# Kernel optimization log

Measured on AMD Instinct MI355X. Metric: run time of the kernel, lower is better.

Reference implementation:

```python
import jax, jax.numpy as jnp
import numpy as np

TOP_K = 2
EPS = 1e-20


def setup_inputs() -> dict:
    key = jax.random.key(0)
    ks = jax.random.split(key, 8)
    B, S, H, E, D = 4, 2048, 1024, 8, 2048
    s = 0.02
    return {
        "x":  jax.random.normal(ks[0], (B, S, H), dtype=jnp.float32),
        "Wr": jax.random.normal(ks[1], (H, E), dtype=jnp.float32) * s,
        "Wg": jax.random.normal(ks[2], (E, H, D), dtype=jnp.float32) * s,
        "Wu": jax.random.normal(ks[3], (E, H, D), dtype=jnp.float32) * s,
        "Wd": jax.random.normal(ks[4], (E, D, H), dtype=jnp.float32) * s,
        "Sg": jax.random.normal(ks[5], (H, D), dtype=jnp.float32) * s,
        "Su": jax.random.normal(ks[6], (H, D), dtype=jnp.float32) * s,
        "Sd": jax.random.normal(ks[7], (D, H), dtype=jnp.float32) * s,
    }


def reference(x, Wr, Wg, Wu, Wd, Sg, Su, Sd):
    B, S, H = x.shape
    T = B * S
    xt = x.reshape(T, H)

    # Router: softmax scores, top-k, renormalize top-k weights
    scores = jax.nn.softmax(xt @ Wr, axis=-1)            # [T, E]
    topk_w, topk_idx = jax.lax.top_k(scores, TOP_K)      # [T, K]
    topk_w = topk_w / (topk_w.sum(axis=-1, keepdims=True) + EPS)

    # Per-expert SwiGLU FFN computed densely over all tokens (vectorized over E)
    g = jax.nn.silu(jnp.einsum('th,ehd->etd', xt, Wg))   # [E, T, D]
    u = jnp.einsum('th,ehd->etd', xt, Wu)                # [E, T, D]
    out_all = jnp.einsum('etd,edh->eth', g * u, Wd)      # [E, T, H]

    # Combine: gather each token's top-k expert outputs, weighted sum
    tok = jnp.arange(T)[:, None]                          # [T, 1]
    gathered = out_all[topk_idx, tok, :]                  # [T, K, H]
    out = jnp.sum(gathered * topk_w[..., None], axis=1).reshape(B, S, H)

    # Shared expert (applied to original input, added to MoE output)
    shared = (jax.nn.silu(x @ Sg) * (x @ Su)) @ Sd        # [B, S, H]
    return out + shared
```

## Files before the change

kernel.cpp:

```cpp
#include <hip/hip_runtime.h>
#include <stdint.h>

#define T_TOK 8192
#define HD 1024
#define ED 8
#define DD 2048
#define BM 128
#define BK 32
#define TILE_SHARED 64
#define TILE_MAX 200
#define ROWCAP 25600
#define RT_TPW 8

typedef short short8 __attribute__((ext_vector_type(8)));
typedef unsigned short ushort8 __attribute__((ext_vector_type(8)));
typedef float f32x4 __attribute__((ext_vector_type(4)));

__device__ __forceinline__ unsigned short f2bf(float f) {
  union { float f; unsigned int u; } v; v.f = f;
  unsigned int r = (v.u + 0x7fffu + ((v.u >> 16) & 1u)) >> 16;
  return (unsigned short)r;
}

__device__ __forceinline__ void gll16(const void* g, void* l) {
  __builtin_amdgcn_global_load_lds(
      (const __attribute__((address_space(1))) unsigned int*)g,
      (__attribute__((address_space(3))) unsigned int*)l, 16, 0, 0);
}

__global__ __launch_bounds__(256) void k_zero(float* __restrict__ outp) {
  size_t i = (size_t)blockIdx.x * 256 + threadIdx.x;
  ((float4*)outp)[i] = make_float4(0.f, 0.f, 0.f, 0.f);
}

__global__ __launch_bounds__(256) void k_init(int* counts, int* tok, float* wrow) {
  int i = blockIdx.x * 256 + threadIdx.x;
  if (i < 32) counts[i] = 0;
  if (i < ROWCAP) {
    tok[i] = (i < T_TOK) ? i : 0;
    wrow[i] = (i < T_TOK) ? 1.0f : 0.0f;
  }
}

__global__ __launch_bounds__(256) void k_transpose(const float* __restrict__ in,
    unsigned short* __restrict__ outp, int R, int C) {
  __shared__ float tile[64][65];
  size_t boff = (size_t)blockIdx.z * (size_t)R * (size_t)C;
  in += boff; outp += boff;
  int c0 = blockIdx.x * 64, r0 = blockIdx.y * 64;
  int tid = threadIdx.x;
  int lr = tid >> 4;
  int lc = (tid & 15) << 2;
#pragma unroll
  for (int p = 0; p < 4; ++p) {
    int row = lr + p * 16;
    float4 v = *(const float4*)&in[(size_t)(r0 + row) * C + c0 + lc];
    tile[row][lc] = v.x; tile[row][lc + 1] = v.y;
    tile[row][lc + 2] = v.z; tile[row][lc + 3] = v.w;
  }
  __syncthreads();
  int cc = tid >> 2;
#pragma unroll
  for (int p = 0; p < 2; ++p) {
    int g = (tid & 3) + p * 4;
    int rr = g * 8;
    ushort8 v;
#pragma unroll
    for (int q = 0; q < 8; ++q) v[q] = f2bf(tile[rr + q][cc]);
    *(ushort8*)&outp[(size_t)(c0 + cc) * R + r0 + rr] = v;
  }
}

__global__ __launch_bounds__(256) void k_router(const float* __restrict__ x,
    const float* __restrict__ Wr, unsigned short* __restrict__ xb,
    int* __restrict__ counts, int* __restrict__ topE, float* __restrict__ topW) {
  __shared__ float wrT[ED * HD];
  __shared__ int hist[ED];
  int tid = threadIdx.x;
  if (tid < ED) hist[tid] = 0;
  for (int i = tid; i < ED * HD; i += 256) {
    int e = i >> 10, h = i & (HD - 1);
    wrT[i] = Wr[h * ED + e];
  }
  __syncthreads();
  int lane = tid & 63, wave = tid >> 6;
  int tbase = (blockIdx.x * 4 + wave) * RT_TPW;
  for (int tt = 0; tt < RT_TPW; ++tt) {
    int t = tbase + tt;
    const float* xrow = x + (size_t)t * HD;
    unsigned short* xbrow = xb + (size_t)t * HD;
    float acc[ED] = {0, 0, 0, 0, 0, 0, 0, 0};
#pragma unroll
    for (int i = 0; i < HD / 64; ++i) {
      int h = i * 64 + lane;
      float v = xrow[h];
      xbrow[h] = f2bf(v);
#pragma unroll
      for (int e = 0; e < ED; ++e) acc[e] += v * wrT[e * HD + h];
    }
#pragma unroll
    for (int off = 32; off; off >>= 1)
#pragma unroll
      for (int e = 0; e < ED; ++e) acc[e] += __shfl_xor(acc[e], off);
    if (lane == 0) {
      float m = acc[0];
#pragma unroll
      for (int e = 1; e < ED; ++e) m = fmaxf(m, acc[e]);
      float p[ED], s = 0.f;
#pragma unroll
      for (int e = 0; e < ED; ++e) { p[e] = __expf(acc[e] - m); s += p[e]; }
      int i0 = 0;
#pragma unroll
      for (int e = 1; e < ED; ++e) if (acc[e] > acc[i0]) i0 = e;
      int i1 = -1;
#pragma unroll
      for (int e = 0; e < ED; ++e) {
        if (e == i0) continue;
        if (i1 < 0 || acc[e] > acc[i1]) i1 = e;
      }
      float p0 = p[i0] / s, p1 = p[i1] / s;
      float rs = p0 + p1 + 1e-20f;
      topE[t * 2] = i0; topE[t * 2 + 1] = i1;
      topW[t * 2] = p0 / rs; topW[t * 2 + 1] = p1 / rs;
      atomicAdd(&hist[i0], 1);
      atomicAdd(&hist[i1], 1);
    }
  }
  __syncthreads();
  if (tid < ED) atomicAdd(&counts[tid], hist[tid]);
}

__global__ __launch_bounds__(256) void k_plan(const int* __restrict__ counts, int* cursor,
    int* __restrict__ tileE, int* __restrict__ tileEnd) {
  __shared__ int tstart[ED + 1], segend[ED];
  if (threadIdx.x == 0) {
    int base = T_TOK, rt = TILE_SHARED;
    for (int e = 0; e < ED; ++e) {
      int c = counts[e];
      cursor[e] = base;
      tstart[e] = rt;
      segend[e] = base + c;
      int tiles = (c + BM - 1) >> 7;
      rt += tiles;
      base += tiles << 7;
    }
    tstart[ED] = rt;
  }
  __syncthreads();
  for (int rt = threadIdx.x; rt < TILE_MAX; rt += 256) {
    int e = -1, end = 0;
    if (rt < TILE_SHARED) { e = ED; end = T_TOK; }
    else {
      for (int q = 0; q < ED; ++q)
        if (rt >= tstart[q] && rt < tstart[q + 1]) { e = q; end = segend[q]; }
    }
    tileE[rt] = e; tileEnd[rt] = end;
  }
}

__global__ __launch_bounds__(256) void k_scatter(const int* __restrict__ topE,
    const float* __restrict__ topW, int* cursor, int* tok, float* wrow) {
  __shared__ int lcount[ED], lbase[ED];
  int tid = threadIdx.x;
  if (tid < ED) lcount[tid] = 0;
  __syncthreads();
  int t = blockIdx.x * 256 + tid;
  int e0 = topE[t * 2], e1 = topE[t * 2 + 1];
  float w0 = topW[t * 2], w1 = topW[t * 2 + 1];
  int s0 = atomicAdd(&lcount[e0], 1);
  int s1 = atomicAdd(&lcount[e1], 1);
  __syncthreads();
  if (tid < ED) lbase[tid] = atomicAdd(&cursor[tid], lcount[tid]);
  __syncthreads();
  int p0 = lbase[e0] + s0;
  int p1 = lbase[e1] + s1;
  tok[p0] = t; wrow[p0] = w0;
  tok[p1] = t; wrow[p1] = w1;
}


__global__ __launch_bounds__(256, 3) void k_gemm1(
    const unsigned short* __restrict__ xb,
    const unsigned short* __restrict__ wgt, const unsigned short* __restrict__ wut,
    const unsigned short* __restrict__ sgt, const unsigned short* __restrict__ sut,
    const int* __restrict__ tok, const int* __restrict__ tileE,
    const int* __restrict__ tileEnd, unsigned short* __restrict__ hbuf, int tileBase) {
  int lin = blockIdx.y * 32 + blockIdx.x;
  int q = (32 * gridDim.y) >> 3;
  int wk = (lin & 7) * q + (lin >> 3);
  int bx = wk & 31, by = wk >> 5;

  int lt = by;
  int rt = tileBase + lt;
  int e = tileE[rt];
  if (e < 0) return;
  int n0 = bx * 64;
  int grow0 = rt * BM;
  int hrow0 = lt * BM;
  int segEnd = tileEnd[rt];
  const unsigned short* bg = (e == ED) ? sgt : wgt + (size_t)e * DD * HD;
  const unsigned short* bu = (e == ED) ? sut : wut + (size_t)e * DD * HD;

  __shared__ __align__(16) unsigned short As[3][BM * BK];
  __shared__ __align__(16) unsigned short Bg[3][64 * BK];
  __shared__ __align__(16) unsigned short Bu[3][64 * BK];

  int tid = threadIdx.x, lane = tid & 63, wave = tid >> 6;
  int wm = (wave & 1) * 64, wn = (wave >> 1) * 32;
  int kc = (lane & 3) ^ ((lane >> 3) & 3);
  int rl = lane >> 2;

  int ldsA[2];
  const unsigned short* pA[2];
#pragma unroll
  for (int r = 0; r < 2; ++r) {
    int chunk = r * 4 + wave;
    ldsA[r] = chunk * 512;
    pA[r] = xb + (size_t)tok[grow0 + chunk * 16 + rl] * HD + kc * 8;
  }
  const unsigned short* pG = bg + (size_t)(n0 + wave * 16 + rl) * HD + kc * 8;
  const unsigned short* pU = bu + (size_t)(n0 + wave * 16 + rl) * HD + kc * 8;
  int dB = wave * 512;

  f32x4 zero = {0.f, 0.f, 0.f, 0.f};
  f32x4 accg[4][2], accu[4][2];
#pragma unroll
  for (int i = 0; i < 4; ++i)
#pragma unroll
    for (int j = 0; j < 2; ++j) { accg[i][j] = zero; accu[i][j] = zero; }

  int m15 = lane & 15;
  int sl8 = (((lane >> 4) ^ ((lane >> 1) & 3)) * 8);

  gll16(pA[0],      &As[0][ldsA[0]]);
  gll16(pA[1],      &As[0][ldsA[1]]);
  gll16(pG,         &Bg[0][dB]);
  gll16(pU,         &Bu[0][dB]);
  __builtin_amdgcn_sched_barrier(0);
  gll16(pA[0] + BK, &As[1][ldsA[0]]);
  gll16(pA[1] + BK, &As[1][ldsA[1]]);
  gll16(pG + BK,    &Bg[1][dB]);
  gll16(pU + BK,    &Bu[1][dB]);

  const int NT = HD / BK;
  for (int t = 0; t < NT; ++t) {
    int b = t % 3;
    if (t + 1 < NT) asm volatile("s_waitcnt vmcnt(4)" ::: "memory");
    else            asm volatile("s_waitcnt vmcnt(0)" ::: "memory");
    __builtin_amdgcn_sched_barrier(0);
    __builtin_amdgcn_s_barrier();
    __builtin_amdgcn_sched_barrier(0);
    int k2 = (t + 2) * BK;
    if (k2 < HD) {
      int b2 = (t + 2) % 3;
      gll16(pA[0] + k2, &As[b2][ldsA[0]]);
      gll16(pA[1] + k2, &As[b2][ldsA[1]]);
      gll16(pG + k2,    &Bg[b2][dB]);
      gll16(pU + k2,    &Bu[b2][dB]);
    }
    __builtin_amdgcn_sched_barrier(0);
    short8 af[4], bgf[2], buf_[2];
#pragma unroll
    for (int i = 0; i < 4; ++i)
      af[i] = *(const short8*)(&As[b][(wm + i * 16 + m15) * BK + sl8]);
#pragma unroll
    for (int j = 0; j < 2; ++j) {
      bgf[j]  = *(const short8*)(&Bg[b][(wn + j * 16 + m15) * BK + sl8]);
      buf_[j] = *(const short8*)(&Bu[b][(wn + j * 16 + m15) * BK + sl8]);
    }
#pragma unroll
    for (int i = 0; i < 4; ++i)
#pragma unroll
      for (int j = 0; j < 2; ++j) {
        accg[i][j] = __builtin_amdgcn_mfma_f32_16x16x32_bf16(af[i], bgf[j],  accg[i][j], 0, 0, 0);
        accu[i][j] = __builtin_amdgcn_mfma_f32_16x16x32_bf16(af[i], buf_[j], accu[i][j], 0, 0, 0);
      }
    __builtin_amdgcn_sched_barrier(0);
  }

  int colB = n0 + wn + m15;
  int rowB = wm + ((lane >> 4) << 2);
#pragma unroll
  for (int i = 0; i < 4; ++i)
#pragma unroll
    for (int j = 0; j < 2; ++j)
#pragma unroll
      for (int r = 0; r < 4; ++r) {
        int lr = rowB + i * 16 + r;
        float g = accg[i][j][r], u = accu[i][j][r];
        float h = (grow0 + lr < segEnd) ? (g / (1.0f + __expf(-g))) * u : 0.0f;
        hbuf[(size_t)(hrow0 + lr) * DD + colB + j * 16] = f2bf(h);
      }
}

__global__ __launch_bounds__(256, 3) void k_gemm2(
    const unsigned short* __restrict__ hbuf,
    const unsigned short* __restrict__ wdt, const unsigned short* __restrict__ sdt,
    const int* __restrict__ tok, const int* __restrict__ tileE,
    const int* __restrict__ tileEnd, const float* __restrict__ wrow,
    float* __restrict__ outp, int tileBase) {
  int lin = blockIdx.y * 8 + blockIdx.x;
  int q = (8 * gridDim.y) >> 3;
  int wk = (lin & 7) * q + (lin >> 3);
  int bx = wk & 7, by = wk >> 3;

  int lt = by;
  int rt = tileBase + lt;
  int e = tileE[rt];
  if (e < 0) return;
  int n0 = bx * BM;
  int grow0 = rt * BM;
  int hrow0 = lt * BM;
  int segEnd = tileEnd[rt];
  const unsigned short* bd = (e == ED) ? sdt : wdt + (size_t)e * HD * DD;

  __shared__ __align__(16) unsigned short As[3][BM * BK];
  __shared__ __align__(16) unsigned short Bs[3][BM * BK];

  int tid = threadIdx.x, lane = tid & 63, wave = tid >> 6;
  int wm = (wave & 1) * 64, wn = (wave >> 1) * 64;
  int kc = (lane & 3) ^ ((lane >> 3) & 3);

  int ldsU[2];
  const unsigned short *pA[2], *pB[2];
#pragma unroll
  for (int r = 0; r < 2; ++r) {
    int chunk = r * 4 + wave;
    int row = chunk * 16 + (lane >> 2);
    ldsU[r] = chunk * 512;
    pA[r] = hbuf + (size_t)(hrow0 + row) * DD + kc * 8;
    pB[r] = bd + (size_t)(n0 + row) * DD + kc * 8;
  }

  f32x4 zero = {0.f, 0.f, 0.f, 0.f};
  f32x4 acc[4][4];
#pragma unroll
  for (int i = 0; i < 4; ++i)
#pragma unroll
    for (int j = 0; j < 4; ++j) acc[i][j] = zero;

  int m15 = lane & 15;
  int sl8 = (((lane >> 4) ^ ((lane >> 1) & 3)) * 8);

#pragma unroll
  for (int r = 0; r < 2; ++r) {
    gll16(pA[r], &As[0][ldsU[r]]);
    gll16(pB[r], &Bs[0][ldsU[r]]);
  }
#pragma unroll
  for (int r = 0; r < 2; ++r) {
    gll16(pA[r] + BK, &As[1][ldsU[r]]);
    gll16(pB[r] + BK, &Bs[1][ldsU[r]]);
  }

  for (int k0 = 0; k0 < DD; k0 += BK) {
    int ti = k0 >> 5;
    int b  = ti % 3;
    if (k0 + BK < DD) asm volatile("s_waitcnt vmcnt(4)" ::: "memory");
    else              asm volatile("s_waitcnt vmcnt(0)" ::: "memory");
    __builtin_amdgcn_sched_barrier(0);
    __builtin_amdgcn_s_barrier();
    __builtin_amdgcn_sched_barrier(0);
    int k2 = k0 + 2 * BK;
    if (k2 < DD) {
      int b2 = (ti + 2) % 3;
#pragma unroll
      for (int r = 0; r < 2; ++r) {
        gll16(pA[r] + k2, &As[b2][ldsU[r]]);
        gll16(pB[r] + k2, &Bs[b2][ldsU[r]]);
      }
    }
    __builtin_amdgcn_sched_barrier(0);
    short8 af[4], bf[4];
#pragma unroll
    for (int i = 0; i < 4; ++i) {
      af[i] = *(const short8*)(&As[b][(wm + i * 16 + m15) * BK + sl8]);
      bf[i] = *(const short8*)(&Bs[b][(wn + i * 16 + m15) * BK + sl8]);
    }
#pragma unroll
    for (int i = 0; i < 4; ++i)
#pragma unroll
      for (int j = 0; j < 4; ++j)
        acc[i][j] = __builtin_amdgcn_mfma_f32_16x16x32_bf16(af[i], bf[j], acc[i][j], 0, 0, 0);
    __builtin_amdgcn_sched_barrier(0);
  }

  int colB = n0 + wn + m15;
  int rowB = wm + ((lane >> 4) << 2);
#pragma unroll
  for (int i = 0; i < 4; ++i)
#pragma unroll
    for (int r = 0; r < 4; ++r) {
      int grr = grow0 + rowB + i * 16 + r;
      if (grr < segEnd) {
        float w = wrow[grr];
        size_t ob = (size_t)tok[grr] * HD;
#pragma unroll
        for (int j = 0; j < 4; ++j)
          atomicAdd(&outp[ob + colB + j * 16], acc[i][j][r] * w);
      }
    }
}

extern "C" void kernel_launch(void* const* d_in, const int* in_sizes, int n_in,
                              void* d_out, int out_size, void* d_ws, size_t ws_size,
                              hipStream_t stream) {
  const float* x  = (const float*)d_in[0];
  const float* Wr = (const float*)d_in[1];
  const float* Wg = (const float*)d_in[2];
  const float* Wu = (const float*)d_in[3];
  const float* Wd = (const float*)d_in[4];
  const float* Sg = (const float*)d_in[5];
  const float* Su = (const float*)d_in[6];
  const float* Sd = (const float*)d_in[7];
  float* outp = (float*)d_out;

  size_t fixed = 0;
  auto pad = [](size_t b) { return (b + 255) & ~(size_t)255; };
  fixed += pad((size_t)T_TOK * HD * 2);
  fixed += pad((size_t)ED * DD * HD * 2) * 3;
  fixed += pad((size_t)DD * HD * 2) * 3;
  fixed += pad((size_t)ROWCAP * 4) * 2;
  fixed += pad((size_t)T_TOK * 2 * 4) * 2;
  fixed += pad(128) * 2 + pad(1024) * 2;
  int CH = TILE_MAX;
  if (fixed + pad((size_t)CH * BM * DD * 2) > ws_size) CH = TILE_MAX / 2;
  if (fixed + pad((size_t)CH * BM * DD * 2) > ws_size) return;

  char* ws = (char*)d_ws;
  size_t off = 0;
  auto alloc = [&](size_t bytes) -> char* {
    char* p = ws + off;
    off += (bytes + 255) & ~(size_t)255;
    return p;
  };
  unsigned short* xb  = (unsigned short*)alloc((size_t)T_TOK * HD * 2);
  unsigned short* wgt = (unsigned short*)alloc((size_t)ED * DD * HD * 2);
  unsigned short* wut = (unsigned short*)alloc((size_t)ED * DD * HD * 2);
  unsigned short* wdt = (unsigned short*)alloc((size_t)ED * HD * DD * 2);
  unsigned short* sgt = (unsigned short*)alloc((size_t)DD * HD * 2);
  unsigned short* sut = (unsigned short*)alloc((size_t)DD * HD * 2);
  unsigned short* sdt = (unsigned short*)alloc((size_t)HD * DD * 2);
  int* tok       = (int*)alloc((size_t)ROWCAP * 4);
  float* wrow    = (float*)alloc((size_t)ROWCAP * 4);
  int* topE      = (int*)alloc((size_t)T_TOK * 2 * 4);
  float* topW    = (float*)alloc((size_t)T_TOK * 2 * 4);
  int* counts    = (int*)alloc(128);
  int* cursor    = (int*)alloc(128);
  int* tileE     = (int*)alloc(1024);
  int* tileEnd   = (int*)alloc(1024);
  unsigned short* hbuf = (unsigned short*)alloc((size_t)CH * BM * DD * 2);

  k_zero<<<(out_size / 4 + 255) / 256, 256, 0, stream>>>(outp);
  k_init<<<(ROWCAP + 255) / 256, 256, 0, stream>>>(counts, tok, wrow);
  k_transpose<<<dim3(DD / 64, HD / 64, ED), 256, 0, stream>>>(Wg, wgt, HD, DD);
  k_transpose<<<dim3(DD / 64, HD / 64, ED), 256, 0, stream>>>(Wu, wut, HD, DD);
  k_transpose<<<dim3(HD / 64, DD / 64, ED), 256, 0, stream>>>(Wd, wdt, DD, HD);
  k_transpose<<<dim3(DD / 64, HD / 64, 1), 256, 0, stream>>>(Sg, sgt, HD, DD);
  k_transpose<<<dim3(DD / 64, HD / 64, 1), 256, 0, stream>>>(Su, sut, HD, DD);
  k_transpose<<<dim3(HD / 64, DD / 64, 1), 256, 0, stream>>>(Sd, sdt, DD, HD);
  k_router<<<T_TOK / (4 * RT_TPW), 256, 0, stream>>>(x, Wr, xb, counts, topE, topW);
  k_plan<<<1, 256, 0, stream>>>(counts, cursor, tileE, tileEnd);
  k_scatter<<<T_TOK / 256, 256, 0, stream>>>(topE, topW, cursor, tok, wrow);
  for (int cb = 0; cb < TILE_MAX; cb += CH) {
    k_gemm1<<<dim3(DD / 64, CH), 256, 0, stream>>>(xb, wgt, wut, sgt, sut, tok,
                                                   tileE, tileEnd, hbuf, cb);
    k_gemm2<<<dim3(HD / BM, CH), 256, 0, stream>>>(hbuf, wdt, sdt, tok, tileE,
                                                   tileEnd, wrow, outp, cb);
  }
}
```

Measured before the change: 767.3 us.

## Replace atomic scatter-add in down-projection with partial buffer and combine kernel

The down-projection epilogue now writes plain stores: shared-expert tiles store directly into the output and routed-expert rows store into a per-row partial buffer. A new combine kernel then adds each token's two routed partials into the output, so the zero-fill kernel and float atomics are no longer needed. The scatter kernel also records each token's row positions. The blockIdx swizzle used for L2 grouping is removed from both GEMMs. The cost is extra workspace and an additional read/write pass over the output, and correctness depends on the shared tiles being written before gemm2 runs for routed tiles.

```diff
diff --git a/kernel.cpp b/kernel.cpp
--- a/kernel.cpp
+++ b/kernel.cpp
@@ -159,7 +159,8 @@
 }
 
 __global__ __launch_bounds__(256) void k_scatter(const int* __restrict__ topE,
-    const float* __restrict__ topW, int* cursor, int* tok, float* wrow) {
+    const float* __restrict__ topW, int* cursor, int* tok, float* wrow,
+    int* __restrict__ rowIdx) {
   __shared__ int lcount[ED], lbase[ED];
   int tid = threadIdx.x;
   if (tid < ED) lcount[tid] = 0;
@@ -176,6 +177,7 @@
   int p1 = lbase[e1] + s1;
   tok[p0] = t; wrow[p0] = w0;
   tok[p1] = t; wrow[p1] = w1;
+  rowIdx[t * 2] = p0; rowIdx[t * 2 + 1] = p1;
 }
 
 
@@ -185,16 +187,11 @@
     const unsigned short* __restrict__ sgt, const unsigned short* __restrict__ sut,
     const int* __restrict__ tok, const int* __restrict__ tileE,
     const int* __restrict__ tileEnd, unsigned short* __restrict__ hbuf, int tileBase) {
-  int lin = blockIdx.y * 32 + blockIdx.x;
-  int q = (32 * gridDim.y) >> 3;
-  int wk = (lin & 7) * q + (lin >> 3);
-  int bx = wk & 31, by = wk >> 5;
-
-  int lt = by;
+  int lt = blockIdx.y;
   int rt = tileBase + lt;
   int e = tileE[rt];
   if (e < 0) return;
-  int n0 = bx * 64;
+  int n0 = blockIdx.x * 64;
   int grow0 = rt * BM;
   int hrow0 = lt * BM;
   int segEnd = tileEnd[rt];
@@ -298,17 +295,12 @@
     const unsigned short* __restrict__ wdt, const unsigned short* __restrict__ sdt,
     const int* __restrict__ tok, const int* __restrict__ tileE,
     const int* __restrict__ tileEnd, const float* __restrict__ wrow,
-    float* __restrict__ outp, int tileBase) {
-  int lin = blockIdx.y * 8 + blockIdx.x;
-  int q = (8 * gridDim.y) >> 3;
-  int wk = (lin & 7) * q + (lin >> 3);
-  int bx = wk & 7, by = wk >> 3;
-
-  int lt = by;
+    float* __restrict__ outp, float* __restrict__ part, int tileBase) {
+  int lt = blockIdx.y;
   int rt = tileBase + lt;
   int e = tileE[rt];
   if (e < 0) return;
-  int n0 = bx * BM;
+  int n0 = blockIdx.x * BM;
   int grow0 = rt * BM;
   int hrow0 = lt * BM;
   int segEnd = tileEnd[rt];
@@ -387,19 +379,62 @@
 
   int colB = n0 + wn + m15;
   int rowB = wm + ((lane >> 4) << 2);
-#pragma unroll
-  for (int i = 0; i < 4; ++i)
-#pragma unroll
-    for (int r = 0; r < 4; ++r) {
-      int grr = grow0 + rowB + i * 16 + r;
-      if (grr < segEnd) {
-        float w = wrow[grr];
-        size_t ob = (size_t)tok[grr] * HD;
-#pragma unroll
-        for (int j = 0; j < 4; ++j)
-          atomicAdd(&outp[ob + colB + j * 16], acc[i][j][r] * w);
+  if (part) {
+    if (e == ED) {
+#pragma unroll
+      for (int i = 0; i < 4; ++i)
+#pragma unroll
+        for (int r = 0; r < 4; ++r) {
+          int grr = grow0 + rowB + i * 16 + r;
+          float w = wrow[grr];
+          size_t ob = (size_t)tok[grr] * HD;
+#pragma unroll
+          for (int j = 0; j < 4; ++j)
+            outp[ob + colB + j * 16] = acc[i][j][r] * w;
+        }
+    } else {
+#pragma unroll
+      for (int i = 0; i < 4; ++i)
+#pragma unroll
+        for (int r = 0; r < 4; ++r) {
+          int grr = grow0 + rowB + i * 16 + r;
+          if (grr < segEnd) {
+            float w = wrow[grr];
+            size_t pb = (size_t)(grr - T_TOK) * HD;
+#pragma unroll
+            for (int j = 0; j < 4; ++j)
+              part[pb + colB + j * 16] = acc[i][j][r] * w;
+          }
+        }
+    }
+  } else {
+#pragma unroll
+    for (int i = 0; i < 4; ++i)
+#pragma unroll
+      for (int r = 0; r < 4; ++r) {
+        int grr = grow0 + rowB + i * 16 + r;
+        if (grr < segEnd) {
+          float w = wrow[grr];
+          size_t ob = (size_t)tok[grr] * HD;
+#pragma unroll
+          for (int j = 0; j < 4; ++j)
+            atomicAdd(&outp[ob + colB + j * 16], acc[i][j][r] * w);
+        }
       }
-    }
+  }
+}
+
+__global__ __launch_bounds__(256) void k_combine(const float* __restrict__ part,
+    const int* __restrict__ rowIdx, float* __restrict__ outp) {
+  int t = blockIdx.x;
+  int c = threadIdx.x;
+  size_t p0 = (size_t)(rowIdx[t * 2]     - T_TOK) * HD;
+  size_t p1 = (size_t)(rowIdx[t * 2 + 1] - T_TOK) * HD;
+  float4 a = ((float4*)(outp + (size_t)t * HD))[c];
+  float4 b = ((const float4*)(part + p0))[c];
+  float4 d = ((const float4*)(part + p1))[c];
+  a.x += b.x + d.x; a.y += b.y + d.y; a.z += b.z + d.z; a.w += b.w + d.w;
+  ((float4*)(outp + (size_t)t * HD))[c] = a;
 }
 
 extern "C" void kernel_launch(void* const* d_in, const int* in_sizes, int n_in,
@@ -415,16 +450,20 @@
   const float* Sd = (const float*)d_in[7];
   float* outp = (float*)d_out;
 
+  auto pad = [](size_t b) { return (b + 255) & ~(size_t)255; };
   size_t fixed = 0;
-  auto pad = [](size_t b) { return (b + 255) & ~(size_t)255; };
   fixed += pad((size_t)T_TOK * HD * 2);
   fixed += pad((size_t)ED * DD * HD * 2) * 3;
   fixed += pad((size_t)DD * HD * 2) * 3;
   fixed += pad((size_t)ROWCAP * 4) * 2;
-  fixed += pad((size_t)T_TOK * 2 * 4) * 2;
+  fixed += pad((size_t)T_TOK * 2 * 4) * 3;
   fixed += pad(128) * 2 + pad(1024) * 2;
+
+  size_t partBytes = (size_t)(ROWCAP - T_TOK) * HD * 4;
   int CH = TILE_MAX;
-  if (fixed + pad((size_t)CH * BM * DD * 2) > ws_size) CH = TILE_MAX / 2;
+  bool usePart = true;
+  if (fixed + pad((size_t)CH * BM * DD * 2) + pad(partBytes) > ws_size) CH = TILE_MAX / 2;
+  if (fixed + pad((size_t)CH * BM * DD * 2) + pad(partBytes) > ws_size) usePart = false;
   if (fixed + pad((size_t)CH * BM * DD * 2) > ws_size) return;
 
   char* ws = (char*)d_ws;
@@ -445,13 +484,16 @@
   float* wrow    = (float*)alloc((size_t)ROWCAP * 4);
   int* topE      = (int*)alloc((size_t)T_TOK * 2 * 4);
   float* topW    = (float*)alloc((size_t)T_TOK * 2 * 4);
+  int* rowIdx    = (int*)alloc((size_t)T_TOK * 2 * 4);
   int* counts    = (int*)alloc(128);
   int* cursor    = (int*)alloc(128);
   int* tileE     = (int*)alloc(1024);
   int* tileEnd   = (int*)alloc(1024);
   unsigned short* hbuf = (unsigned short*)alloc((size_t)CH * BM * DD * 2);
-
-  k_zero<<<(out_size / 4 + 255) / 256, 256, 0, stream>>>(outp);
+  float* part = usePart ? (float*)alloc(partBytes) : nullptr;
+
+  if (!usePart)
+    k_zero<<<(out_size / 4 + 255) / 256, 256, 0, stream>>>(outp);
   k_init<<<(ROWCAP + 255) / 256, 256, 0, stream>>>(counts, tok, wrow);
   k_transpose<<<dim3(DD / 64, HD / 64, ED), 256, 0, stream>>>(Wg, wgt, HD, DD);
   k_transpose<<<dim3(DD / 64, HD / 64, ED), 256, 0, stream>>>(Wu, wut, HD, DD);
@@ -461,11 +503,13 @@
   k_transpose<<<dim3(HD / 64, DD / 64, 1), 256, 0, stream>>>(Sd, sdt, DD, HD);
   k_router<<<T_TOK / (4 * RT_TPW), 256, 0, stream>>>(x, Wr, xb, counts, topE, topW);
   k_plan<<<1, 256, 0, stream>>>(counts, cursor, tileE, tileEnd);
-  k_scatter<<<T_TOK / 256, 256, 0, stream>>>(topE, topW, cursor, tok, wrow);
+  k_scatter<<<T_TOK / 256, 256, 0, stream>>>(topE, topW, cursor, tok, wrow, rowIdx);
   for (int cb = 0; cb < TILE_MAX; cb += CH) {
     k_gemm1<<<dim3(DD / 64, CH), 256, 0, stream>>>(xb, wgt, wut, sgt, sut, tok,
                                                    tileE, tileEnd, hbuf, cb);
     k_gemm2<<<dim3(HD / BM, CH), 256, 0, stream>>>(hbuf, wdt, sdt, tok, tileE,
-                                                   tileEnd, wrow, outp, cb);
-  }
-}
+                                                   tileEnd, wrow, outp, part, cb);
+  }
+  if (usePart)
+    k_combine<<<T_TOK, 256, 0, stream>>>(part, rowIdx, outp);
+}
```

New measurement: 770.2 us. Within noise of the previous version (+0.4%).
